# Kernel tuning notes

Measured on AMD Instinct MI355X. Metric: run time of the kernel, lower is better.

The kernel has to match this reference:

```python
import jax, jax.numpy as jnp
import numpy as np

N = 50000
E = 800000
IN_DIM, HID, LAT, DEC_HID = 256, 256, 128, 512


def _glorot(key, shape):
    fan_in, fan_out = shape
    lim = np.sqrt(6.0 / (fan_in + fan_out))
    return jax.random.uniform(key, shape, jnp.float32, -lim, lim)


def setup_inputs() -> dict:
    key = jax.random.key(0)
    ks = jax.random.split(key, 10)
    x = jax.random.normal(ks[0], (N, IN_DIM), jnp.float32)
    edge_index = jax.random.randint(ks[1], (2, E), 0, N, dtype=jnp.int64)
    return {
        "x": x,
        "edge_index": edge_index,
        "W1": _glorot(ks[2], (IN_DIM, HID)), "b1": jnp.zeros((HID,), jnp.float32),
        "W2": _glorot(ks[3], (HID, LAT)), "b2": jnp.zeros((LAT,), jnp.float32),
        "Wd1": _glorot(ks[4], (LAT, DEC_HID)), "bd1": jnp.zeros((DEC_HID,), jnp.float32),
        "Wd2": _glorot(ks[5], (DEC_HID, IN_DIM)), "bd2": jnp.zeros((IN_DIM,), jnp.float32),
    }


def _gcn_layer(x, src, dst, W, b, num_nodes):
    # linear transform
    xt = x @ W + b                      # [N, out]
    # scatter-mean aggregation over incoming edges (PyG aggr='mean')
    msg = xt[src]                       # [E, out] gather of source features
    summed = jax.ops.segment_sum(msg, dst, num_segments=num_nodes)
    cnt = jax.ops.segment_sum(jnp.ones((src.shape[0],), xt.dtype), dst,
                              num_segments=num_nodes)
    mean = summed / jnp.maximum(cnt, 1.0)[:, None]   # 0 for isolated nodes
    # relu + residual
    return jax.nn.relu(mean) + xt


def reference(x, edge_index, W1, b1, W2, b2, Wd1, bd1, Wd2, bd2):
    src, dst = edge_index[0], edge_index[1]
    h = _gcn_layer(x, src, dst, W1, b1, x.shape[0])
    z = _gcn_layer(h, src, dst, W2, b2, x.shape[0])
    # decoder MLP
    x_hat = jax.nn.relu(z @ Wd1 + bd1) @ Wd2 + bd2
    return (x_hat, z)
```

## Files before the change

### kernel.cpp

```cpp
#include <hip/hip_runtime.h>
#include <hip/hip_bf16.h>

#define TPB 256

typedef __attribute__((ext_vector_type(8))) short short8;
typedef __attribute__((ext_vector_type(4))) float f32x4;

__device__ __forceinline__ unsigned short f2bf(float f) {
    unsigned int u = __float_as_uint(f);
    u = (u + 0x7FFFu + ((u >> 16) & 1u)) >> 16;
    return (unsigned short)u;
}
__device__ __forceinline__ float bflo(unsigned int u) { return __uint_as_float(u << 16); }
__device__ __forceinline__ float bfhi(unsigned int u) { return __uint_as_float(u & 0xFFFF0000u); }

__device__ __forceinline__ void gload16(const void* g, void* l) {
    __builtin_amdgcn_global_load_lds(
        (const __attribute__((address_space(1))) unsigned int*)g,
        (__attribute__((address_space(3))) unsigned int*)l, 16, 0, 0);
}

__global__ void transpose_convert_all(
    const float* __restrict__ Wa, unsigned short* __restrict__ Ta, int Ka, int Na,
    const float* __restrict__ Wb, unsigned short* __restrict__ Tb, int Kb, int Nb,
    const float* __restrict__ Wc, unsigned short* __restrict__ Tc, int Kc, int Nc_,
    const float* __restrict__ Wd, unsigned short* __restrict__ Td, int Kd, int Nd)
{
    __shared__ float tile[32][33];
    int b = blockIdx.x;
    const float* W; unsigned short* T; int K, Nn;
    const int ta = (Na / 32) * (Ka / 32);
    const int tb = (Nb / 32) * (Kb / 32);
    const int tc = (Nc_ / 32) * (Kc / 32);
    if (b < ta)                { W = Wa; T = Ta; K = Ka; Nn = Na; }
    else if (b < ta + tb)      { b -= ta;           W = Wb; T = Tb; K = Kb; Nn = Nb; }
    else if (b < ta + tb + tc) { b -= ta + tb;      W = Wc; T = Tc; K = Kc; Nn = Nc_; }
    else                       { b -= ta + tb + tc; W = Wd; T = Td; K = Kd; Nn = Nd; }
    const int nx = Nn / 32;
    const int n0 = (b % nx) * 32;
    const int k0 = (b / nx) * 32;
    const int tx = threadIdx.x, ty = threadIdx.y;
#pragma unroll
    for (int i = 0; i < 4; ++i)
        tile[ty + i * 8][tx] = W[(size_t)(k0 + ty + i * 8) * Nn + n0 + tx];
    __syncthreads();
#pragma unroll
    for (int i = 0; i < 4; ++i)
        T[(size_t)(n0 + ty + i * 8) * K + k0 + tx] = f2bf(tile[tx][ty + i * 8]);
}

__device__ __forceinline__ void load_a16f(const float* p, short8& lo, short8& hi) {
    float4 f0 = *reinterpret_cast<const float4*>(p);
    float4 f1 = *reinterpret_cast<const float4*>(p + 4);
    float4 f2 = *reinterpret_cast<const float4*>(p + 8);
    float4 f3 = *reinterpret_cast<const float4*>(p + 12);
    lo[0] = (short)f2bf(f0.x); lo[1] = (short)f2bf(f0.y);
    lo[2] = (short)f2bf(f0.z); lo[3] = (short)f2bf(f0.w);
    lo[4] = (short)f2bf(f1.x); lo[5] = (short)f2bf(f1.y);
    lo[6] = (short)f2bf(f1.z); lo[7] = (short)f2bf(f1.w);
    hi[0] = (short)f2bf(f2.x); hi[1] = (short)f2bf(f2.y);
    hi[2] = (short)f2bf(f2.z); hi[3] = (short)f2bf(f2.w);
    hi[4] = (short)f2bf(f3.x); hi[5] = (short)f2bf(f3.y);
    hi[6] = (short)f2bf(f3.z); hi[7] = (short)f2bf(f3.w);
}

__device__ __forceinline__ void copy_out32(unsigned short* C, const float* Cst, const float* bias,
                                           int rowbase, int bn, int M, int Nc, int t, bool doRelu) {
#pragma unroll
    for (int it = 0; it < 2; ++it) {
        const int idx = it * 2048 + t * 8;
        const int row = idx >> 7, col = idx & 127;
        const int m = rowbase + row;
        if (m >= M) continue;
        float4 v0 = *reinterpret_cast<const float4*>(&Cst[idx]);
        float4 v1 = *reinterpret_cast<const float4*>(&Cst[idx + 4]);
        float4 b0 = *reinterpret_cast<const float4*>(&bias[bn + col]);
        float4 b1 = *reinterpret_cast<const float4*>(&bias[bn + col + 4]);
        float o[8] = {v0.x + b0.x, v0.y + b0.y, v0.z + b0.z, v0.w + b0.w,
                      v1.x + b1.x, v1.y + b1.y, v1.z + b1.z, v1.w + b1.w};
        short8 s;
#pragma unroll
        for (int j = 0; j < 8; ++j) {
            const float vv = doRelu ? fmaxf(o[j], 0.f) : o[j];
            s[j] = (short)f2bf(vv);
        }
        *reinterpret_cast<short8*>(&C[(size_t)m * Nc + bn + col]) = s;
    }
}
__device__ __forceinline__ void copy_out32(float* C, const float* Cst, const float* bias,
                                           int rowbase, int bn, int M, int Nc, int t, bool doRelu) {
#pragma unroll
    for (int it = 0; it < 4; ++it) {
        const int idx = it * 1024 + t * 4;
        const int row = idx >> 7, col = idx & 127;
        const int m = rowbase + row;
        if (m >= M) continue;
        float4 v = *reinterpret_cast<const float4*>(&Cst[idx]);
        float4 b = *reinterpret_cast<const float4*>(&bias[bn + col]);
        v.x += b.x; v.y += b.y; v.z += b.z; v.w += b.w;
        if (doRelu) {
            v.x = fmaxf(v.x, 0.f); v.y = fmaxf(v.y, 0.f);
            v.z = fmaxf(v.z, 0.f); v.w = fmaxf(v.w, 0.f);
        }
        *reinterpret_cast<float4*>(&C[(size_t)m * Nc + bn + col]) = v;
    }
}

template <typename TA, typename TC, int K, bool RELU>
__global__ __launch_bounds__(256) void mfma_gemm3(
    const TA* __restrict__ A, const unsigned short* __restrict__ Bt,
    const float* __restrict__ bias, TC* __restrict__ C, int M, int Nc)
{
    __shared__ unsigned short lds_s[12288];
    constexpr bool AF32 = (sizeof(TA) == 4);

    const int t  = threadIdx.x;
    const int l  = t & 63;
    const int w  = t >> 6;
    const int wm = w >> 1, wn = w & 1;
    const int bm = blockIdx.x * 64;
    const int bn = blockIdx.y * 128;

    f32x4 acc[2][4] = {};

    const int r4 = t >> 2;
    const int q4 = t & 3;
    const int gmr = bm + r4;
    short8 sa0, sa1;

    auto loadAregs = [&](int k0) {
        if (gmr < M) load_a16f((const float*)A + (size_t)gmr * K + k0 + q4 * 16, sa0, sa1);
        else { sa0 = (short8)0; sa1 = (short8)0; }
    };
    auto writeAregs = [&]() {
        const int s0 = (2 * q4)     ^ (r4 & 7);
        const int s1 = (2 * q4 + 1) ^ (r4 & 7);
        *reinterpret_cast<short8*>(&lds_s[r4 * 64 + s0 * 8]) = sa0;
        *reinterpret_cast<short8*>(&lds_s[r4 * 64 + s1 * 8]) = sa1;
    };
    auto stageA_lds = [&](int k0) {
#pragma unroll
        for (int ii = 0; ii < 2; ++ii) {
            const int seg = w + ii * 4;
            const int rr  = seg * 8 + (l >> 3);
            const int ss  = l & 7;
            const int gr  = min(bm + rr, M - 1);
            gload16((const unsigned short*)A + (size_t)gr * K + k0 + ((ss ^ (rr & 7)) * 8),
                    &lds_s[seg * 512]);
        }
    };
    auto stageB = [&](int k0) {
#pragma unroll
        for (int ii = 0; ii < 4; ++ii) {
            const int seg = w + ii * 4;
            const int rr  = seg * 8 + (l >> 3);
            const int ss  = l & 7;
            gload16(Bt + (size_t)(bn + rr) * K + k0 + ((ss ^ (rr & 7)) * 8),
                    &lds_s[4096 + seg * 512]);
        }
    };

    if (AF32) loadAregs(0);

    constexpr int S = K / 64;
#pragma unroll
    for (int step = 0; step < S; ++step) {
        const int k0 = step * 64;
        if (AF32) writeAregs(); else stageA_lds(k0);
        stageB(k0);
        __syncthreads();
        if (AF32 && step + 1 < S) loadAregs(k0 + 64);

#pragma unroll
        for (int kk = 0; kk < 2; ++kk) {
            short8 af[2], bf4[4];
#pragma unroll
            for (int mf = 0; mf < 2; ++mf) {
                const int row  = wm * 32 + mf * 16 + (l & 15);
                const int slot = (kk * 4 + (l >> 4)) ^ (row & 7);
                af[mf] = *reinterpret_cast<const short8*>(&lds_s[row * 64 + slot * 8]);
            }
#pragma unroll
            for (int nf = 0; nf < 4; ++nf) {
                const int row  = wn * 64 + nf * 16 + (l & 15);
                const int slot = (kk * 4 + (l >> 4)) ^ (row & 7);
                bf4[nf] = *reinterpret_cast<const short8*>(&lds_s[4096 + row * 64 + slot * 8]);
            }
#pragma unroll
            for (int mf = 0; mf < 2; ++mf)
#pragma unroll
                for (int nf = 0; nf < 4; ++nf)
                    acc[mf][nf] = __builtin_amdgcn_mfma_f32_16x16x32_bf16(
                        af[mf], bf4[nf], acc[mf][nf], 0, 0, 0);
        }
        __syncthreads();
    }

    float* Cst = reinterpret_cast<float*>(lds_s);
#pragma unroll
    for (int p = 0; p < 2; ++p) {
        if (wm == p) {
#pragma unroll
            for (int mf = 0; mf < 2; ++mf)
#pragma unroll
                for (int nf = 0; nf < 4; ++nf)
#pragma unroll
                    for (int rr = 0; rr < 4; ++rr) {
                        const int row = mf * 16 + (l >> 4) * 4 + rr;
                        const int col = wn * 64 + nf * 16 + (l & 15);
                        Cst[row * 128 + col] = acc[mf][nf][rr];
                    }
        }
        __syncthreads();
        copy_out32(C, Cst, bias, bm + p * 32, bn, M, Nc, t, RELU);
        if (p == 0) __syncthreads();
    }
}

__global__ void hist_kernel(const int* __restrict__ dst, int* __restrict__ counts, int E)
{
    int e = blockIdx.x * TPB + threadIdx.x;
    if (e < E) atomicAdd(&counts[dst[e]], 1);
}

__global__ void scan1_kernel(const int* __restrict__ counts,
                             int* __restrict__ local, int* __restrict__ bsum, int N)
{
    __shared__ int sh[TPB];
    const int t = threadIdx.x;
    const int base = blockIdx.x * 1024 + t * 4;
    int v[4];
#pragma unroll
    for (int i = 0; i < 4; ++i) v[i] = (base + i < N) ? counts[base + i] : 0;
    const int s = v[0] + v[1] + v[2] + v[3];
    sh[t] = s;
    __syncthreads();
    for (int d = 1; d < TPB; d <<= 1) {
        int x = (t >= d) ? sh[t - d] : 0;
        __syncthreads();
        sh[t] += x;
        __syncthreads();
    }
    int run = sh[t] - s;
#pragma unroll
    for (int i = 0; i < 4; ++i) {
        if (base + i < N) local[base + i] = run;
        run += v[i];
    }
    if (t == TPB - 1) bsum[blockIdx.x] = sh[TPB - 1];
}

__global__ void scan2_kernel(int* __restrict__ bsum, int nb)
{
    __shared__ int sh[TPB];
    const int t = threadIdx.x;
    const int v = (t < nb) ? bsum[t] : 0;
    sh[t] = v;
    __syncthreads();
    for (int d = 1; d < TPB; d <<= 1) {
        int x = (t >= d) ? sh[t - d] : 0;
        __syncthreads();
        sh[t] += x;
        __syncthreads();
    }
    if (t < nb) bsum[t] = sh[t] - v;
}

__global__ void scan3_kernel(int* __restrict__ offsets, int* __restrict__ cursor,
                             const int* __restrict__ bsum, int N)
{
    const int i = blockIdx.x * TPB + threadIdx.x;
    if (i < N) {
        const int o = offsets[i] + bsum[i >> 10];
        offsets[i] = o;
        cursor[i]  = o;
    }
}

__global__ void build_perm_kernel(const int* __restrict__ src, const int* __restrict__ dst,
                                  int* __restrict__ cursor, int* __restrict__ perm, int E)
{
    int e = blockIdx.x * TPB + threadIdx.x;
    if (e < E) {
        int pos = atomicAdd(&cursor[dst[e]], 1);
        perm[pos] = src[e];
    }
}

template <int F, int CH, bool WRITE_ZF32>
__global__ __launch_bounds__(256) void agg_kernel(
    const uint2* __restrict__ xt,
    const int* __restrict__ offsets, const int* __restrict__ counts,
    const int* __restrict__ perm,
    uint2* __restrict__ out, float* __restrict__ zf32, int N)
{
    constexpr int RU  = F / 4;
    constexpr int L   = RU / CH;
    constexpr int NPB = TPB / L;

    const int chunk = blockIdx.x % CH;
    const int node  = (blockIdx.x / CH) * NPB + threadIdx.x / L;
    const int g     = threadIdx.x % L;
    if (node >= N) return;
    const int col = chunk * L + g;

    const int start = offsets[node];
    const int deg   = counts[node];

    float a0 = 0.f, a1 = 0.f, a2 = 0.f, a3 = 0.f;

    for (int base = 0; base < deg; base += L) {
        const int m = min(L, deg - base);
        const int pidx = perm[start + base + ((g < m) ? g : (m - 1))];
        int j = 0;
        for (; j + 4 <= m; j += 4) {
            const int s0 = __shfl(pidx, j + 0, L);
            const int s1 = __shfl(pidx, j + 1, L);
            const int s2 = __shfl(pidx, j + 2, L);
            const int s3 = __shfl(pidx, j + 3, L);
            const uint2 v0 = xt[(size_t)s0 * RU + col];
            const uint2 v1 = xt[(size_t)s1 * RU + col];
            const uint2 v2 = xt[(size_t)s2 * RU + col];
            const uint2 v3 = xt[(size_t)s3 * RU + col];
            a0 += bflo(v0.x) + bflo(v1.x) + bflo(v2.x) + bflo(v3.x);
            a1 += bfhi(v0.x) + bfhi(v1.x) + bfhi(v2.x) + bfhi(v3.x);
            a2 += bflo(v0.y) + bflo(v1.y) + bflo(v2.y) + bflo(v3.y);
            a3 += bfhi(v0.y) + bfhi(v1.y) + bfhi(v2.y) + bfhi(v3.y);
        }
        for (; j < m; ++j) {
            const int s = __shfl(pidx, j, L);
            const uint2 v = xt[(size_t)s * RU + col];
            a0 += bflo(v.x); a1 += bfhi(v.x);
            a2 += bflo(v.y); a3 += bfhi(v.y);
        }
    }

    const float c = (float)max(deg, 1);
    const uint2 xv = xt[(size_t)node * RU + col];
    const float r0 = fmaxf(a0 / c, 0.f) + bflo(xv.x);
    const float r1 = fmaxf(a1 / c, 0.f) + bfhi(xv.x);
    const float r2 = fmaxf(a2 / c, 0.f) + bflo(xv.y);
    const float r3 = fmaxf(a3 / c, 0.f) + bfhi(xv.y);

    uint2 o;
    o.x = (unsigned int)f2bf(r0) | ((unsigned int)f2bf(r1) << 16);
    o.y = (unsigned int)f2bf(r2) | ((unsigned int)f2bf(r3) << 16);
    out[(size_t)node * RU + col] = o;
    if (WRITE_ZF32) {
        float4 z4 = make_float4(r0, r1, r2, r3);
        *reinterpret_cast<float4*>(&zf32[(size_t)node * F + 4 * col]) = z4;
    }
}

extern "C" void kernel_launch(void* const* d_in, const int* in_sizes, int n_in,
                              void* d_out, int out_size, void* d_ws, size_t ws_size,
                              hipStream_t stream)
{
    const int IN_DIM = 256, HID = 256, LAT = 128, DEC_HID = 512;
    const int N = in_sizes[0] / IN_DIM;
    const int E = in_sizes[1] / 2;

    const float* x   = (const float*)d_in[0];
    const int*   ei  = (const int*)d_in[1];
    const float* W1  = (const float*)d_in[2];
    const float* b1  = (const float*)d_in[3];
    const float* W2  = (const float*)d_in[4];
    const float* b2  = (const float*)d_in[5];
    const float* Wd1 = (const float*)d_in[6];
    const float* bd1 = (const float*)d_in[7];
    const float* Wd2 = (const float*)d_in[8];
    const float* bd2 = (const float*)d_in[9];

    const int* src = ei;
    const int* dst = ei + E;

    unsigned short* xt1  = (unsigned short*)d_ws;
    unsigned short* h    = xt1  + (size_t)N * 256;
    unsigned short* xt2  = h    + (size_t)N * 256;
    unsigned short* zbf  = xt2  + (size_t)N * 128;
    unsigned short* hdec = zbf  + (size_t)N * 128;
    unsigned short* wt1  = hdec + (size_t)N * 512;
    unsigned short* wt2  = wt1  + 256 * 256;
    unsigned short* wtd1 = wt2  + 128 * 256;
    unsigned short* wtd2 = wtd1 + 512 * 128;
    int* counts  = (int*)(wtd2 + 256 * 512);
    int* offsets = counts + N;
    int* cursor  = offsets + N;
    int* bsum    = cursor + N;
    int* perm    = bsum + 256;

    float* out_xhat = (float*)d_out;
    float* out_z    = out_xhat + (size_t)N * IN_DIM;

    dim3 blk(TPB);
    const int egrid = (E + TPB - 1) / TPB;
    const int mb64 = (N + 63) / 64;
    const int nscan = (N + 1023) / 1024;

    {
        const int tiles = (HID/32)*(IN_DIM/32) + (LAT/32)*(HID/32)
                        + (DEC_HID/32)*(LAT/32) + (IN_DIM/32)*(DEC_HID/32);
        transpose_convert_all<<<tiles, dim3(32, 8), 0, stream>>>(
            W1, wt1, IN_DIM, HID,  W2, wt2, HID, LAT,
            Wd1, wtd1, LAT, DEC_HID,  Wd2, wtd2, DEC_HID, IN_DIM);
    }

    hipMemsetAsync(counts, 0, (size_t)N * 4, stream);
    hist_kernel<<<egrid, blk, 0, stream>>>(dst, counts, E);
    scan1_kernel<<<nscan, blk, 0, stream>>>(counts, offsets, bsum, N);
    scan2_kernel<<<1, blk, 0, stream>>>(bsum, nscan);
    scan3_kernel<<<(N + TPB - 1) / TPB, blk, 0, stream>>>(offsets, cursor, bsum, N);
    build_perm_kernel<<<egrid, blk, 0, stream>>>(src, dst, cursor, perm, E);

    mfma_gemm3<float, unsigned short, 256, false><<<dim3(mb64, HID / 128), blk, 0, stream>>>(
        x, wt1, b1, xt1, N, HID);
    {
        const int ngroups = (N + 15) / 16;
        agg_kernel<256, 4, false><<<ngroups * 4, blk, 0, stream>>>(
            (const uint2*)xt1, offsets, counts, perm, (uint2*)h, nullptr, N);
    }

    mfma_gemm3<unsigned short, unsigned short, 256, false><<<dim3(mb64, LAT / 128), blk, 0, stream>>>(
        h, wt2, b2, xt2, N, LAT);
    {
        const int ngroups = (N + 7) / 8;
        agg_kernel<128, 1, true><<<ngroups, blk, 0, stream>>>(
            (const uint2*)xt2, offsets, counts, perm, (uint2*)zbf, out_z, N);
    }

    mfma_gemm3<unsigned short, unsigned short, 128, true><<<dim3(mb64, DEC_HID / 128), blk, 0, stream>>>(
        zbf, wtd1, bd1, hdec, N, DEC_HID);
    mfma_gemm3<unsigned short, float, 512, false><<<dim3(mb64, IN_DIM / 128), blk, 0, stream>>>(
        hdec, wtd2, bd2, out_xhat, N, IN_DIM);
}
```

Baseline: 276.1 us.

## Double-buffer LDS tiles in MFMA GEMM to overlap loads with compute

```diff
diff --git a/kernel.cpp b/kernel.cpp
--- a/kernel.cpp
+++ b/kernel.cpp
@@ -107,11 +107,11 @@
 }
 
 template <typename TA, typename TC, int K, bool RELU>
-__global__ __launch_bounds__(256) void mfma_gemm3(
+__global__ __launch_bounds__(256) void mfma_gemm4(
     const TA* __restrict__ A, const unsigned short* __restrict__ Bt,
     const float* __restrict__ bias, TC* __restrict__ C, int M, int Nc)
 {
-    __shared__ unsigned short lds_s[12288];
+    __shared__ unsigned short lds_s[2][12288];
     constexpr bool AF32 = (sizeof(TA) == 4);
 
     const int t  = threadIdx.x;
@@ -132,13 +132,13 @@
         if (gmr < M) load_a16f((const float*)A + (size_t)gmr * K + k0 + q4 * 16, sa0, sa1);
         else { sa0 = (short8)0; sa1 = (short8)0; }
     };
-    auto writeAregs = [&]() {
+    auto writeAregs = [&](int buf) {
         const int s0 = (2 * q4)     ^ (r4 & 7);
         const int s1 = (2 * q4 + 1) ^ (r4 & 7);
-        *reinterpret_cast<short8*>(&lds_s[r4 * 64 + s0 * 8]) = sa0;
-        *reinterpret_cast<short8*>(&lds_s[r4 * 64 + s1 * 8]) = sa1;
+        *reinterpret_cast<short8*>(&lds_s[buf][r4 * 64 + s0 * 8]) = sa0;
+        *reinterpret_cast<short8*>(&lds_s[buf][r4 * 64 + s1 * 8]) = sa1;
     };
-    auto stageA_lds = [&](int k0) {
+    auto stageA_lds = [&](int buf, int k0) {
 #pragma unroll
         for (int ii = 0; ii < 2; ++ii) {
             const int seg = w + ii * 4;
@@ -146,30 +146,43 @@
             const int ss  = l & 7;
             const int gr  = min(bm + rr, M - 1);
             gload16((const unsigned short*)A + (size_t)gr * K + k0 + ((ss ^ (rr & 7)) * 8),
-                    &lds_s[seg * 512]);
+                    &lds_s[buf][seg * 512]);
         }
     };
-    auto stageB = [&](int k0) {
+    auto stageB = [&](int buf, int k0) {
 #pragma unroll
         for (int ii = 0; ii < 4; ++ii) {
             const int seg = w + ii * 4;
             const int rr  = seg * 8 + (l >> 3);
             const int ss  = l & 7;
             gload16(Bt + (size_t)(bn + rr) * K + k0 + ((ss ^ (rr & 7)) * 8),
-                    &lds_s[4096 + seg * 512]);
+                    &lds_s[buf][4096 + seg * 512]);
         }
     };
 
-    if (AF32) loadAregs(0);
-
     constexpr int S = K / 64;
+
+    if (AF32) {
+        loadAregs(0);
+        writeAregs(0);
+        if (S > 1) loadAregs(64);
+    } else {
+        stageA_lds(0, 0);
+    }
+    stageB(0, 0);
+    __syncthreads();
+
 #pragma unroll
     for (int step = 0; step < S; ++step) {
-        const int k0 = step * 64;
-        if (AF32) writeAregs(); else stageA_lds(k0);
-        stageB(k0);
-        __syncthreads();
-        if (AF32 && step + 1 < S) loadAregs(k0 + 64);
+        const int k0  = step * 64;
+        const int cur = step & 1;
+
+        if (step + 1 < S) {
+            if (AF32) writeAregs(cur ^ 1);
+            else      stageA_lds(cur ^ 1, k0 + 64);
+            stageB(cur ^ 1, k0 + 64);
+        }
+        if (AF32 && step + 2 < S) loadAregs(k0 + 128);
 
 #pragma unroll
         for (int kk = 0; kk < 2; ++kk) {
@@ -178,13 +191,13 @@
             for (int mf = 0; mf < 2; ++mf) {
                 const int row  = wm * 32 + mf * 16 + (l & 15);
                 const int slot = (kk * 4 + (l >> 4)) ^ (row & 7);
-                af[mf] = *reinterpret_cast<const short8*>(&lds_s[row * 64 + slot * 8]);
+                af[mf] = *reinterpret_cast<const short8*>(&lds_s[cur][row * 64 + slot * 8]);
             }
 #pragma unroll
             for (int nf = 0; nf < 4; ++nf) {
                 const int row  = wn * 64 + nf * 16 + (l & 15);
                 const int slot = (kk * 4 + (l >> 4)) ^ (row & 7);
-                bf4[nf] = *reinterpret_cast<const short8*>(&lds_s[4096 + row * 64 + slot * 8]);
+                bf4[nf] = *reinterpret_cast<const short8*>(&lds_s[cur][4096 + row * 64 + slot * 8]);
             }
 #pragma unroll
             for (int mf = 0; mf < 2; ++mf)
@@ -412,7 +425,7 @@
     scan3_kernel<<<(N + TPB - 1) / TPB, blk, 0, stream>>>(offsets, cursor, bsum, N);
     build_perm_kernel<<<egrid, blk, 0, stream>>>(src, dst, cursor, perm, E);
 
-    mfma_gemm3<float, unsigned short, 256, false><<<dim3(mb64, HID / 128), blk, 0, stream>>>(
+    mfma_gemm4<float, unsigned short, 256, false><<<dim3(mb64, HID / 128), blk, 0, stream>>>(
         x, wt1, b1, xt1, N, HID);
     {
         const int ngroups = (N + 15) / 16;
@@ -420,7 +433,7 @@
             (const uint2*)xt1, offsets, counts, perm, (uint2*)h, nullptr, N);
     }
 
-    mfma_gemm3<unsigned short, unsigned short, 256, false><<<dim3(mb64, LAT / 128), blk, 0, stream>>>(
+    mfma_gemm4<unsigned short, unsigned short, 256, false><<<dim3(mb64, LAT / 128), blk, 0, stream>>>(
         h, wt2, b2, xt2, N, LAT);
     {
         const int ngroups = (N + 7) / 8;
@@ -428,8 +441,8 @@
             (const uint2*)xt2, offsets, counts, perm, (uint2*)zbf, out_z, N);
     }
 
-    mfma_gemm3<unsigned short, unsigned short, 128, true><<<dim3(mb64, DEC_HID / 128), blk, 0, stream>>>(
+    mfma_gemm4<unsigned short, unsigned short, 128, true><<<dim3(mb64, DEC_HID / 128), blk, 0, stream>>>(
         zbf, wtd1, bd1, hdec, N, DEC_HID);
-    mfma_gemm3<unsigned short, float, 512, false><<<dim3(mb64, IN_DIM / 128), blk, 0, stream>>>(
+    mfma_gemm4<unsigned short, float, 512, false><<<dim3(mb64, IN_DIM / 128), blk, 0, stream>>>(
         hdec, wtd2, bd2, out_xhat, N, IN_DIM);
 }
```

New measurement: 277.7 us. About the same (+0.6%).
